# Kernel tuning notes

Measured on AMD Instinct MI355X. Metric: run time of the kernel, lower is better.

## Reference

```python
import jax, jax.numpy as jnp
import numpy as np

B, S, D, H = 4, 2048, 1024, 16
HD = D // H  # head dim = 64


def setup_inputs() -> dict:
    key = jax.random.key(0)
    ks = jax.random.split(key, 9)
    scale = 1.0 / np.sqrt(D)
    inputs = jax.random.normal(ks[0], (B, S, D), dtype=jnp.float32)
    # causal lower-triangular mask, dim==2 -> broadcast [1,1,S,S] in self-attention branch
    mask = jnp.tril(jnp.ones((S, S), dtype=bool))
    Wq = jax.random.normal(ks[1], (D, D), dtype=jnp.float32) * scale
    bq = jnp.zeros((D,), dtype=jnp.float32)
    Wk = jax.random.normal(ks[2], (D, D), dtype=jnp.float32) * scale
    bk = jnp.zeros((D,), dtype=jnp.float32)
    Wv = jax.random.normal(ks[3], (D, D), dtype=jnp.float32) * scale
    bv = jnp.zeros((D,), dtype=jnp.float32)
    Wo = jax.random.normal(ks[4], (D, D), dtype=jnp.float32) * scale
    bo = jnp.zeros((D,), dtype=jnp.float32)
    return {"inputs": inputs, "mask": mask, "Wq": Wq, "bq": bq, "Wk": Wk,
            "bk": bk, "Wv": Wv, "bv": bv, "Wo": Wo, "bo": bo}


def reference(inputs, mask, Wq, bq, Wk, bk, Wv, bv, Wo, bo):
    # Dropout is identity in eval mode (reference baseline).
    b, s, _ = inputs.shape
    q = (inputs @ Wq.T + bq).reshape(b, s, H, HD).transpose(0, 2, 1, 3)  # [b,h,s,hd]
    k = (inputs @ Wk.T + bk).reshape(b, s, H, HD).transpose(0, 2, 1, 3)
    v = (inputs @ Wv.T + bv).reshape(b, s, H, HD).transpose(0, 2, 1, 3)
    scores = jnp.einsum('bhqd,bhkd->bhqk', q, k) / jnp.sqrt(jnp.float32(HD))
    scores = jnp.where(mask[None, None, :, :], scores, jnp.float32(-1e9))
    attn = jax.nn.softmax(scores, axis=-1)
    z = jnp.einsum('bhqk,bhkd->bhqd', attn, v)          # [b,h,s,hd]
    z = z.transpose(0, 2, 1, 3).reshape(b, s, H * HD)   # [b,s,D]
    return z @ Wo.T + bo
```

## Files before the change

kernel.cpp:

```cpp
#include <hip/hip_runtime.h>

#define Bn 4
#define Sn 2048
#define Dn 1024
#define Hn 16
#define HDn 64
#define MROWS (Bn * Sn)

typedef __attribute__((ext_vector_type(4))) float f32x4;
typedef __attribute__((ext_vector_type(8))) _Float16 f16x8;
typedef __attribute__((ext_vector_type(4))) _Float16 f16x4;
typedef unsigned int u32;

__device__ inline void gld_lds16(const void* g, void* l) {
    __builtin_amdgcn_global_load_lds(
        (const __attribute__((address_space(1))) u32*)g,
        (__attribute__((address_space(3))) u32*)l, 16, 0, 0);
}

__global__ __launch_bounds__(256)
void w2h(const float* __restrict__ q, const float* __restrict__ k,
         const float* __restrict__ v, const float* __restrict__ o,
         _Float16* __restrict__ out)
{
    const int i = blockIdx.x * 256 + threadIdx.x;
    const float* src = (blockIdx.y == 0) ? q : (blockIdx.y == 1) ? k
                     : (blockIdx.y == 2) ? v : o;
    const float4 x = ((const float4*)src)[i];
    f16x4 h;
    h[0] = (_Float16)x.x; h[1] = (_Float16)x.y;
    h[2] = (_Float16)x.z; h[3] = (_Float16)x.w;
    ((f16x4*)(out + (size_t)blockIdx.y * Dn * Dn))[i] = h;
}

__global__ __launch_bounds__(256)
void gemm_qkv(const float* __restrict__ A, const _Float16* __restrict__ Wh,
              const float* __restrict__ bq, const float* __restrict__ bk,
              const float* __restrict__ bv, _Float16* __restrict__ Qh,
              _Float16* __restrict__ Kh, _Float16* __restrict__ Vt)
{
    __shared__ __align__(16) _Float16 As[128 * 32];
    __shared__ __align__(16) _Float16 Bs[128 * 32];
    const int tid = threadIdx.x;
    const int lane = tid & 63;
    const int w = tid >> 6;
    const int l15 = lane & 15, lg = lane >> 4;
    const int wr = w >> 1, wc = w & 1;
    const int n0 = blockIdx.x * 128, m0 = blockIdx.y * 128;

    f32x4 acc[4][4];
#pragma unroll
    for (int mi = 0; mi < 4; ++mi)
#pragma unroll
        for (int ni = 0; ni < 4; ++ni) acc[mi][ni] = (f32x4){0.f, 0.f, 0.f, 0.f};

    const int brsub = lane >> 2;
    const int bch = (lane & 3) ^ ((lane >> 2) & 3) ^ ((lane >> 4) & 3);
    const int fsw = (l15 & 3) ^ ((l15 >> 2) & 3);

    for (int k0 = 0; k0 < Dn; k0 += 32) {
        __syncthreads();
#pragma unroll
        for (int c = 0; c < 2; ++c) {
            const int rb = (w * 2 + c) * 16;
            const size_t gsrc = (size_t)(n0 + rb + brsub) * Dn + k0 + bch * 8;
            gld_lds16(Wh + gsrc, &Bs[rb * 32]);
        }
#pragma unroll
        for (int it = 0; it < 4; ++it) {
            const int qi = tid + (it << 8);
            const int row = qi >> 3, qc = qi & 7;
            const float4 v = *(const float4*)&A[(size_t)(m0 + row) * Dn + k0 + qc * 4];
            f16x4 h4;
            h4[0] = (_Float16)v.x; h4[1] = (_Float16)v.y;
            h4[2] = (_Float16)v.z; h4[3] = (_Float16)v.w;
            const int sw = (qc >> 1) ^ (row & 3) ^ ((row >> 2) & 3);
            *(f16x4*)&As[row * 32 + sw * 8 + (qc & 1) * 4] = h4;
        }
        __syncthreads();

        f16x8 af[4];
#pragma unroll
        for (int mi = 0; mi < 4; ++mi) {
            const int ar = wr * 64 + mi * 16 + l15;
            af[mi] = *(const f16x8*)&As[ar * 32 + ((lg ^ fsw) << 3)];
        }
#pragma unroll
        for (int ni = 0; ni < 4; ++ni) {
            const int br = wc * 64 + ni * 16 + l15;
            const f16x8 bf = *(const f16x8*)&Bs[br * 32 + ((lg ^ fsw) << 3)];
#pragma unroll
            for (int mi = 0; mi < 4; ++mi)
                acc[mi][ni] = __builtin_amdgcn_mfma_f32_16x16x32_f16(af[mi], bf, acc[mi][ni], 0, 0, 0);
        }
    }

    const int mat = n0 >> 10;
    const float* bias = (mat == 0) ? bq : (mat == 1) ? bk : bv;
#pragma unroll
    for (int ni = 0; ni < 4; ++ni) {
        const int col = n0 + wc * 64 + ni * 16 + l15;
        const int cmod = col & 1023;
        const float bcol = bias[cmod];
        const int hh = cmod >> 6, dd = cmod & 63;
#pragma unroll
        for (int mi = 0; mi < 4; ++mi) {
            const int mb = m0 + wr * 64 + mi * 16 + (lg << 2);
            const int ss = mb & (Sn - 1);
            const int bb = mb >> 11;
            if (mat == 0) {
#pragma unroll
                for (int r = 0; r < 4; ++r) {
                    const size_t ad = ((((size_t)bb * Hn + hh) * Sn + (ss + r)) << 6) + dd;
                    Qh[ad] = (_Float16)((acc[mi][ni][r] + bcol) * 0.125f);
                }
            } else if (mat == 1) {
#pragma unroll
                for (int r = 0; r < 4; ++r) {
                    const size_t ad = ((((size_t)bb * Hn + hh) * Sn + (ss + r)) << 6) + dd;
                    Kh[ad] = (_Float16)(acc[mi][ni][r] + bcol);
                }
            } else {
                f16x4 hv;
                hv[0] = (_Float16)(acc[mi][ni][0] + bcol);
                hv[1] = (_Float16)(acc[mi][ni][1] + bcol);
                hv[2] = (_Float16)(acc[mi][ni][2] + bcol);
                hv[3] = (_Float16)(acc[mi][ni][3] + bcol);
                const size_t ad = (((size_t)bb * Hn + hh) * HDn + dd) * Sn + ss;
                *(f16x4*)&Vt[ad] = hv;
            }
        }
    }
}

__global__ __launch_bounds__(256)
void gemm_out(const float* __restrict__ A, const _Float16* __restrict__ Wh,
              const float* __restrict__ bias, float* __restrict__ Cf)
{
    __shared__ __align__(16) _Float16 Ah[128 * 32];
    __shared__ __align__(16) _Float16 Al[128 * 32];
    __shared__ __align__(16) _Float16 Bs[128 * 32];
    const int tid = threadIdx.x;
    const int lane = tid & 63;
    const int w = tid >> 6;
    const int l15 = lane & 15, lg = lane >> 4;
    const int wr = w >> 1, wc = w & 1;
    const int n0 = blockIdx.x * 128, m0 = blockIdx.y * 128;

    f32x4 acc[4][4];
#pragma unroll
    for (int mi = 0; mi < 4; ++mi)
#pragma unroll
        for (int ni = 0; ni < 4; ++ni) acc[mi][ni] = (f32x4){0.f, 0.f, 0.f, 0.f};

    const int brsub = lane >> 2;
    const int bch = (lane & 3) ^ ((lane >> 2) & 3) ^ ((lane >> 4) & 3);
    const int fsw = (l15 & 3) ^ ((l15 >> 2) & 3);

    for (int k0 = 0; k0 < Dn; k0 += 32) {
        __syncthreads();
#pragma unroll
        for (int c = 0; c < 2; ++c) {
            const int rb = (w * 2 + c) * 16;
            const size_t gsrc = (size_t)(n0 + rb + brsub) * Dn + k0 + bch * 8;
            gld_lds16(Wh + gsrc, &Bs[rb * 32]);
        }
#pragma unroll
        for (int it = 0; it < 4; ++it) {
            const int qi = tid + (it << 8);
            const int row = qi >> 3, qc = qi & 7;
            const float4 v = *(const float4*)&A[(size_t)(m0 + row) * Dn + k0 + qc * 4];
            f16x4 h4, l4;
            h4[0] = (_Float16)v.x; l4[0] = (_Float16)(v.x - (float)h4[0]);
            h4[1] = (_Float16)v.y; l4[1] = (_Float16)(v.y - (float)h4[1]);
            h4[2] = (_Float16)v.z; l4[2] = (_Float16)(v.z - (float)h4[2]);
            h4[3] = (_Float16)v.w; l4[3] = (_Float16)(v.w - (float)h4[3]);
            const int sw = (qc >> 1) ^ (row & 3) ^ ((row >> 2) & 3);
            const int off = row * 32 + sw * 8 + (qc & 1) * 4;
            *(f16x4*)&Ah[off] = h4;
            *(f16x4*)&Al[off] = l4;
        }
        __syncthreads();

        f16x8 ah[4], al[4];
#pragma unroll
        for (int mi = 0; mi < 4; ++mi) {
            const int ar = wr * 64 + mi * 16 + l15;
            const int off = ar * 32 + ((lg ^ fsw) << 3);
            ah[mi] = *(const f16x8*)&Ah[off];
            al[mi] = *(const f16x8*)&Al[off];
        }
#pragma unroll
        for (int ni = 0; ni < 4; ++ni) {
            const int br = wc * 64 + ni * 16 + l15;
            const f16x8 bh = *(const f16x8*)&Bs[br * 32 + ((lg ^ fsw) << 3)];
#pragma unroll
            for (int mi = 0; mi < 4; ++mi) {
                acc[mi][ni] = __builtin_amdgcn_mfma_f32_16x16x32_f16(ah[mi], bh, acc[mi][ni], 0, 0, 0);
                acc[mi][ni] = __builtin_amdgcn_mfma_f32_16x16x32_f16(al[mi], bh, acc[mi][ni], 0, 0, 0);
            }
        }
    }

#pragma unroll
    for (int ni = 0; ni < 4; ++ni) {
        const int col = n0 + wc * 64 + ni * 16 + l15;
        const float bcol = bias[col];
#pragma unroll
        for (int mi = 0; mi < 4; ++mi) {
            const int mb = m0 + wr * 64 + mi * 16 + (lg << 2);
#pragma unroll
            for (int r = 0; r < 4; ++r)
                Cf[(size_t)(mb + r) * Dn + col] = acc[mi][ni][r] + bcol;
        }
    }
}

__device__ inline void stage_half(const _Float16* __restrict__ gp, _Float16* lb,
                                  bool isK, int t0, int half, int rsub, int sch)
{
#pragma unroll
    for (int i = 0; i < 4; ++i) {
        const int row = half * 32 + i * 8 + rsub;
        const _Float16* s_ = isK
            ? (gp + (size_t)(t0 + row) * HDn + sch * 8)
            : (gp + (size_t)row * Sn + t0 + sch * 8);
        gld_lds16(s_, lb + (size_t)(half * 32 + i * 8) * 64);
    }
}

__global__ __launch_bounds__(256, 3)
void attn_fwd(const _Float16* __restrict__ Qh, const _Float16* __restrict__ Kh,
              const _Float16* __restrict__ Vt, float* __restrict__ Z)
{
    __shared__ __align__(16) _Float16 Ks[2][4096];
    __shared__ __align__(16) _Float16 Vs[2][4096];
    __shared__ __align__(16) _Float16 Ps[4][32 * 72];

    const int tid = threadIdx.x, lane = tid & 63, w = tid >> 6;
    const int l15 = lane & 15, lg = lane >> 4;

    const int d  = (int)blockIdx.x;
    const int wu = (d & 7) * 128 + (d >> 3);
    const int qb = 15 - (wu & 15);
    const int h  = (wu >> 4) & 15;
    const int b  = wu >> 8;
    const int q0b = qb << 7;

    const size_t khoff = ((size_t)(b * Hn + h) * Sn) * HDn;
    const size_t vhoff = ((size_t)(b * Hn + h) * HDn) * Sn;
    const _Float16* Qg = Qh + khoff;
    const _Float16* Kg = Kh + khoff;
    const _Float16* Vg = Vt + vhoff;

    const int rsub = lane >> 3;
    const int sch  = (lane & 7) ^ rsub;
    const bool isK = (w < 2);
    const int half = w & 1;
    const _Float16* gp = isK ? Kg : Vg;

    f16x8 qf[2][2];
#pragma unroll
    for (int miq = 0; miq < 2; ++miq) {
        const _Float16* qsrc = &Qg[(size_t)(q0b + w * 32 + miq * 16 + l15) * HDn + lg * 8];
        qf[miq][0] = *(const f16x8*)qsrc;
        qf[miq][1] = *(const f16x8*)(qsrc + 32);
    }

    f32x4 acc[2][4];
#pragma unroll
    for (int miq = 0; miq < 2; ++miq)
#pragma unroll
        for (int nt = 0; nt < 4; ++nt) acc[miq][nt] = (f32x4){0.f, 0.f, 0.f, 0.f};
    float psum[2][4];
#pragma unroll
    for (int miq = 0; miq < 2; ++miq)
#pragma unroll
        for (int r = 0; r < 4; ++r) psum[miq][r] = 0.f;

    _Float16* Pw = &Ps[w][0];
    const int xa = (lg ^ (l15 & 7)) << 3;
    const int xb = ((lg ^ (l15 & 7)) ^ 4) << 3;
    const int qlo_w = q0b + w * 32;
    const int ntiles = 2 * qb + 2;

    stage_half(gp, isK ? &Ks[0][0] : &Vs[0][0], isK, 0, half, rsub, sch);

    for (int t = 0; t < ntiles; ++t) {
        if (t + 1 < ntiles) {
            _Float16* sb = isK ? &Ks[(t & 1) ^ 1][0] : &Vs[(t & 1) ^ 1][0];
            stage_half(gp, sb, isK, (t + 1) << 6, half, rsub, sch);
            asm volatile("s_waitcnt vmcnt(4)" ::: "memory");
        } else {
            asm volatile("s_waitcnt vmcnt(0)" ::: "memory");
        }
        __builtin_amdgcn_s_barrier();
        __builtin_amdgcn_sched_barrier(0);

        const _Float16* Kc = &Ks[t & 1][0];
        const _Float16* Vc = &Vs[t & 1][0];
        const int t0k = t << 6;
        const bool act[2] = { t0k <= qlo_w + 15, t0k <= qlo_w + 31 };
        const bool need_mask = (t0k + 63 > qlo_w);

        f32x4 sv[2][4];
#pragma unroll
        for (int nt = 0; nt < 4; ++nt) {
            const int kr = (nt * 16 + l15) << 6;
            const f16x8 k0 = *(const f16x8*)&Kc[kr + xa];
            const f16x8 k1 = *(const f16x8*)&Kc[kr + xb];
            __builtin_amdgcn_s_setprio(1);
#pragma unroll
            for (int miq = 0; miq < 2; ++miq) {
                if (!act[miq]) continue;
                f32x4 s = (f32x4){0.f, 0.f, 0.f, 0.f};
                s = __builtin_amdgcn_mfma_f32_16x16x32_f16(qf[miq][0], k0, s, 0, 0, 0);
                s = __builtin_amdgcn_mfma_f32_16x16x32_f16(qf[miq][1], k1, s, 0, 0, 0);
                sv[miq][nt] = s;
            }
            __builtin_amdgcn_s_setprio(0);
        }

        if (need_mask) {
#pragma unroll
            for (int miq = 0; miq < 2; ++miq) {
                if (!act[miq]) continue;
#pragma unroll
                for (int nt = 0; nt < 4; ++nt) {
                    const int key = t0k + nt * 16 + l15;
#pragma unroll
                    for (int r = 0; r < 4; ++r) {
                        const int qq = qlo_w + miq * 16 + (lg << 2) + r;
                        if (key > qq) sv[miq][nt][r] = -1e30f;
                    }
                }
            }
        }

#pragma unroll
        for (int miq = 0; miq < 2; ++miq) {
            if (!act[miq]) continue;
#pragma unroll
            for (int nt = 0; nt < 4; ++nt) {
#pragma unroll
                for (int r = 0; r < 4; ++r) {
                    const float p = __expf(fminf(sv[miq][nt][r], 10.f));
                    sv[miq][nt][r] = p;
                    psum[miq][r] += p;
                }
#pragma unroll
                for (int r = 0; r < 4; ++r)
                    Pw[(miq * 16 + (lg << 2) + r) * 72 + nt * 16 + l15] =
                        (_Float16)sv[miq][nt][r];
            }
        }

        f16x8 pa[2][2];
#pragma unroll
        for (int miq = 0; miq < 2; ++miq)
            if (act[miq]) {
                pa[miq][0] = *(const f16x8*)&Pw[(miq * 16 + l15) * 72 + (lg << 3)];
                pa[miq][1] = *(const f16x8*)&Pw[(miq * 16 + l15) * 72 + 32 + (lg << 3)];
            }

#pragma unroll
        for (int nt = 0; nt < 4; ++nt) {
            const int vr = (nt * 16 + l15) << 6;
            const f16x8 v0 = *(const f16x8*)&Vc[vr + xa];
            const f16x8 v1 = *(const f16x8*)&Vc[vr + xb];
            __builtin_amdgcn_s_setprio(1);
#pragma unroll
            for (int miq = 0; miq < 2; ++miq) {
                if (!act[miq]) continue;
                acc[miq][nt] = __builtin_amdgcn_mfma_f32_16x16x32_f16(pa[miq][0], v0, acc[miq][nt], 0, 0, 0);
                acc[miq][nt] = __builtin_amdgcn_mfma_f32_16x16x32_f16(pa[miq][1], v1, acc[miq][nt], 0, 0, 0);
            }
            __builtin_amdgcn_s_setprio(0);
        }

        __builtin_amdgcn_sched_barrier(0);
        __builtin_amdgcn_s_barrier();
    }

#pragma unroll
    for (int miq = 0; miq < 2; ++miq)
#pragma unroll
        for (int r = 0; r < 4; ++r) {
            float rs = psum[miq][r];
            rs += __shfl_xor(rs, 1);
            rs += __shfl_xor(rs, 2);
            rs += __shfl_xor(rs, 4);
            rs += __shfl_xor(rs, 8);
            const float inv = 1.f / rs;
            const int qg = q0b + w * 32 + miq * 16 + (lg << 2) + r;
            float* dst = &Z[(size_t)(b * Sn + qg) * Dn + h * HDn];
#pragma unroll
            for (int nt = 0; nt < 4; ++nt)
                dst[nt * 16 + l15] = acc[miq][nt][r] * inv;
        }
}

extern "C" void kernel_launch(void* const* d_in, const int* in_sizes, int n_in,
                              void* d_out, int out_size, void* d_ws, size_t ws_size,
                              hipStream_t stream)
{
    const float* x  = (const float*)d_in[0];
    const float* Wq = (const float*)d_in[2];
    const float* bq = (const float*)d_in[3];
    const float* Wk = (const float*)d_in[4];
    const float* bk = (const float*)d_in[5];
    const float* Wv = (const float*)d_in[6];
    const float* bv = (const float*)d_in[7];
    const float* Wo = (const float*)d_in[8];
    const float* bo = (const float*)d_in[9];
    float* out = (float*)d_out;

    char* ws = (char*)d_ws;
    float*    Zf  = (float*)ws;
    _Float16* Qh  = (_Float16*)(ws + 33554432);
    _Float16* Kh  = (_Float16*)(ws + 50331648);
    _Float16* VTh = (_Float16*)(ws + 67108864);
    _Float16* Whp = (_Float16*)(ws + 83886080);

    const int wn4 = Dn * Dn / 4;
    const size_t WN = (size_t)Dn * Dn;

    w2h<<<dim3(wn4 / 256, 4), 256, 0, stream>>>(Wq, Wk, Wv, Wo, Whp);
    gemm_qkv<<<dim3(3 * Dn / 128, MROWS / 128), 256, 0, stream>>>(
        x, Whp, bq, bk, bv, Qh, Kh, VTh);

    attn_fwd<<<dim3(1024), 256, 0, stream>>>(Qh, Kh, VTh, Zf);

    gemm_out<<<dim3(Dn / 128, MROWS / 128), 256, 0, stream>>>(
        Zf, Whp + 3 * WN, bo, out);
}
```

Baseline: 246.4 us.

## Pre-convert x to fp16, load GEMM A tiles via LDS DMA, remap blocks by XCD

Adds an x2h kernel that converts the fp32 activations to fp16 once, into workspace space that Zf reuses later. The QKV GEMM then streams both A and B tiles with global_load_lds instead of converting A through registers every k step. The GEMM grid is flattened to 1D and remapped so each XCD handles a contiguous range of tiles, which should improve L2 reuse. The cost is an extra elementwise pass over the input and one more kernel launch.

Result: faster. 234.0 us (-5.0%).

```diff
diff --git a/kernel.cpp b/kernel.cpp
--- a/kernel.cpp
+++ b/kernel.cpp
@@ -34,7 +34,18 @@
 }
 
 __global__ __launch_bounds__(256)
-void gemm_qkv(const float* __restrict__ A, const _Float16* __restrict__ Wh,
+void x2h(const float* __restrict__ in, _Float16* __restrict__ out)
+{
+    const int i = blockIdx.x * 256 + threadIdx.x;
+    const float4 x = ((const float4*)in)[i];
+    f16x4 h;
+    h[0] = (_Float16)x.x; h[1] = (_Float16)x.y;
+    h[2] = (_Float16)x.z; h[3] = (_Float16)x.w;
+    ((f16x4*)out)[i] = h;
+}
+
+__global__ __launch_bounds__(256)
+void gemm_qkv(const _Float16* __restrict__ Ah16, const _Float16* __restrict__ Wh,
               const float* __restrict__ bq, const float* __restrict__ bk,
               const float* __restrict__ bv, _Float16* __restrict__ Qh,
               _Float16* __restrict__ Kh, _Float16* __restrict__ Vt)
@@ -46,7 +57,11 @@
     const int w = tid >> 6;
     const int l15 = lane & 15, lg = lane >> 4;
     const int wr = w >> 1, wc = w & 1;
-    const int n0 = blockIdx.x * 128, m0 = blockIdx.y * 128;
+
+    const int d  = (int)blockIdx.x;
+    const int wu = (d & 7) * 192 + (d >> 3);
+    const int m0 = (wu / 24) * 128;
+    const int n0 = (wu % 24) * 128;
 
     f32x4 acc[4][4];
 #pragma unroll
@@ -54,28 +69,19 @@
 #pragma unroll
         for (int ni = 0; ni < 4; ++ni) acc[mi][ni] = (f32x4){0.f, 0.f, 0.f, 0.f};
 
-    const int brsub = lane >> 2;
-    const int bch = (lane & 3) ^ ((lane >> 2) & 3) ^ ((lane >> 4) & 3);
-    const int fsw = (l15 & 3) ^ ((l15 >> 2) & 3);
+    const int rsub = lane >> 2;
+    const int sch  = (lane & 3) ^ ((lane >> 2) & 3) ^ ((lane >> 4) & 3);
+    const int fsw  = (l15 & 3) ^ ((l15 >> 2) & 3);
 
     for (int k0 = 0; k0 < Dn; k0 += 32) {
         __syncthreads();
 #pragma unroll
-        for (int c = 0; c < 2; ++c) {
-            const int rb = (w * 2 + c) * 16;
-            const size_t gsrc = (size_t)(n0 + rb + brsub) * Dn + k0 + bch * 8;
-            gld_lds16(Wh + gsrc, &Bs[rb * 32]);
-        }
-#pragma unroll
-        for (int it = 0; it < 4; ++it) {
-            const int qi = tid + (it << 8);
-            const int row = qi >> 3, qc = qi & 7;
-            const float4 v = *(const float4*)&A[(size_t)(m0 + row) * Dn + k0 + qc * 4];
-            f16x4 h4;
-            h4[0] = (_Float16)v.x; h4[1] = (_Float16)v.y;
-            h4[2] = (_Float16)v.z; h4[3] = (_Float16)v.w;
-            const int sw = (qc >> 1) ^ (row & 3) ^ ((row >> 2) & 3);
-            *(f16x4*)&As[row * 32 + sw * 8 + (qc & 1) * 4] = h4;
+        for (int i = 0; i < 2; ++i) {
+            const int row = w * 32 + i * 16 + rsub;
+            gld_lds16(Ah16 + (size_t)(m0 + row) * Dn + k0 + sch * 8,
+                      &As[(w * 32 + i * 16) * 32]);
+            gld_lds16(Wh + (size_t)(n0 + row) * Dn + k0 + sch * 8,
+                      &Bs[(w * 32 + i * 16) * 32]);
         }
         __syncthreads();
 
@@ -417,6 +423,7 @@
 
     char* ws = (char*)d_ws;
     float*    Zf  = (float*)ws;
+    _Float16* xh  = (_Float16*)(ws + 16777216);
     _Float16* Qh  = (_Float16*)(ws + 33554432);
     _Float16* Kh  = (_Float16*)(ws + 50331648);
     _Float16* VTh = (_Float16*)(ws + 67108864);
@@ -426,8 +433,8 @@
     const size_t WN = (size_t)Dn * Dn;
 
     w2h<<<dim3(wn4 / 256, 4), 256, 0, stream>>>(Wq, Wk, Wv, Wo, Whp);
-    gemm_qkv<<<dim3(3 * Dn / 128, MROWS / 128), 256, 0, stream>>>(
-        x, Whp, bq, bk, bv, Qh, Kh, VTh);
+    x2h<<<dim3(MROWS * Dn / 4 / 256), 256, 0, stream>>>(x, xh);
+    gemm_qkv<<<dim3(1536), 256, 0, stream>>>(xh, Whp, bq, bk, bv, Qh, Kh, VTh);
 
     attn_fwd<<<dim3(1024), 256, 0, stream>>>(Qh, Kh, VTh, Zf);
 
```
